# Kernel optimization log

Hardware: AMD Instinct MI355X
Metric: run time of the kernel (lower is better)

The kernel has to match this reference:

```python
import jax, jax.numpy as jnp
import numpy as np

N_HEAD = 16


def setup_inputs() -> dict:
    key = jax.random.key(0)
    ks = jax.random.split(key, 5)
    B, T, C = 4, 2048, 1024
    # torch Linear stored as [out,in]; we use [in,out] so x @ W matches x @ W_t.T
    return {
        "x": jax.random.normal(ks[0], (B, T, C), jnp.float32),
        "c_attn_w": jax.random.normal(ks[1], (C, 3 * C), jnp.float32) * 0.02,
        "c_attn_b": jax.random.normal(ks[2], (3 * C,), jnp.float32) * 0.02,
        "c_proj_w": jax.random.normal(ks[3], (C, C), jnp.float32) * 0.02,
        "c_proj_b": jax.random.normal(ks[4], (C,), jnp.float32) * 0.02,
    }


def reference(x, c_attn_w, c_attn_b, c_proj_w, c_proj_b):
    B, T, C = x.shape
    H = N_HEAD
    d = C // H
    qkv = x @ c_attn_w + c_attn_b                      # [B,T,3C]
    q, k, v = jnp.split(qkv, 3, axis=2)
    q = q.reshape(B, T, H, d).transpose(0, 2, 1, 3)    # [B,H,T,d]
    k = k.reshape(B, T, H, d).transpose(0, 2, 1, 3)
    v = v.reshape(B, T, H, d).transpose(0, 2, 1, 3)
    scale = 1.0 / jnp.sqrt(jnp.asarray(d, x.dtype))
    w = jnp.einsum("bhqd,bhkd->bhqk", q, k) * scale    # [B,H,T,T]
    causal = jnp.tril(jnp.ones((T, T), bool))
    w = jnp.where(causal, w, jnp.asarray(-jnp.inf, w.dtype))
    w = jax.nn.softmax(w, axis=-1)
    y = jnp.einsum("bhqk,bhkd->bhqd", w, v)            # [B,H,T,d]
    y = y.transpose(0, 2, 1, 3).reshape(B, T, C)
    return y @ c_proj_w + c_proj_b
```

## Files before the change

kernel.cpp:

```cpp
#include <hip/hip_runtime.h>
#include <hip/hip_bf16.h>
#include <stdint.h>

#define DEV __device__ __forceinline__

typedef __attribute__((ext_vector_type(8))) short short8;
typedef __attribute__((ext_vector_type(8))) _Float16 half8;
typedef __attribute__((ext_vector_type(2))) __fp16 fp16x2;
typedef __attribute__((ext_vector_type(4))) float floatx4;
typedef __attribute__((ext_vector_type(16))) float floatx16;

DEV unsigned short f2bf(float f) {
  union { float f; uint32_t u; } v; v.f = f;
  uint32_t u = v.u;
  u += 0x7fffu + ((u >> 16) & 1u);
  return (unsigned short)(u >> 16);
}
DEV unsigned short f2h(float f) {
  union { _Float16 h; unsigned short u; } c; c.h = (_Float16)f; return c.u;
}
DEV void async_cp16(const unsigned short* g, unsigned short* l) {
  __builtin_amdgcn_global_load_lds(
      (const __attribute__((address_space(1))) uint32_t*)g,
      (__attribute__((address_space(3))) uint32_t*)l, 16, 0, 0);
}

__global__ __launch_bounds__(256)
void cvt_x_kernel(const float* __restrict__ x, unsigned short* __restrict__ xb) {
  const size_t i = ((size_t)blockIdx.x * 256 + threadIdx.x) * 4;
  const float4 f = *(const float4*)(x + i);
  ushort4 w;
  w.x = f2bf(f.x); w.y = f2bf(f.y); w.z = f2bf(f.z); w.w = f2bf(f.w);
  *(ushort4*)(xb + i) = w;
}

__global__ __launch_bounds__(256)
void transpose_w_kernel(const float* __restrict__ W, unsigned short* __restrict__ Wt,
                        int K, int N) {
  __shared__ float tile[64][65];
  const int k0 = blockIdx.y * 64, n0 = blockIdx.x * 64;
  const int tr = threadIdx.x >> 4;
  const int tc = (threadIdx.x & 15) * 4;
#pragma unroll
  for (int it = 0; it < 4; ++it) {
    const int k = tr + it * 16;
    const float4 f = *(const float4*)(W + (size_t)(k0 + k) * N + n0 + tc);
    tile[k][tc + 0] = f.x; tile[k][tc + 1] = f.y;
    tile[k][tc + 2] = f.z; tile[k][tc + 3] = f.w;
  }
  __syncthreads();
#pragma unroll
  for (int it = 0; it < 4; ++it) {
    const int n = tr + it * 16;
    ushort4 w;
    w.x = f2bf(tile[tc + 0][n]); w.y = f2bf(tile[tc + 1][n]);
    w.z = f2bf(tile[tc + 2][n]); w.w = f2bf(tile[tc + 3][n]);
    *(ushort4*)(Wt + (size_t)(n0 + n) * K + k0 + tc) = w;
  }
}

#define BAR asm volatile("s_barrier" ::: "memory")
#define LGK0 asm volatile("s_waitcnt lgkmcnt(0)" ::: "memory")
#define VMW(N) asm volatile("s_waitcnt vmcnt(" #N ")" ::: "memory")
#define NOW (void)0
#define NOSTG (void)0

template <int EPI, int BN>
__global__ __launch_bounds__(512, 2)
void gemm256_kernel(const unsigned short* __restrict__ A,
                    const unsigned short* __restrict__ Bt,
                    const float* __restrict__ bias, int M, int N, int K,
                    int nbx,
                    unsigned short* __restrict__ qws,
                    unsigned short* __restrict__ kws,
                    unsigned short* __restrict__ vws,
                    float* __restrict__ out) {
  (void)M;
  constexpr int NF = BN / 64;
  __shared__ __align__(16) unsigned short L[2][16384 + NF * 4096];
  const int tid = threadIdx.x;
  const int wid = tid >> 6, lane = tid & 63;
  const int quad = lane >> 4, l16 = lane & 15;
  const int wm = wid >> 2, wn = wid & 3;

  const int nwg = (int)gridDim.x;
  const int bid = (int)blockIdx.x;
  const int swz = (bid & 7) * (nwg >> 3) + (bid >> 3);
  const int bx = swz % nbx, by = swz / nbx;
  const int rowA0 = by * 256, colB0 = bx * BN;

  const int srow = tid >> 3;
  const int ksrc = (((tid & 7) ^ (srow & 7)) << 3);
  const unsigned short* pA00 = A + (size_t)(rowA0 + 0   + srow) * K + ksrc;
  const unsigned short* pA01 = A + (size_t)(rowA0 + 64  + srow) * K + ksrc;
  const unsigned short* pA10 = A + (size_t)(rowA0 + 128 + srow) * K + ksrc;
  const unsigned short* pA11 = A + (size_t)(rowA0 + 192 + srow) * K + ksrc;
  const unsigned short* pB00 = Bt + (size_t)(colB0 + 0   + srow) * K + ksrc;
  const unsigned short* pB01 = Bt + (size_t)(colB0 + 64  + srow) * K + ksrc;
  const unsigned short* pB10 =
      (BN == 256) ? Bt + (size_t)(colB0 + 128 + srow) * K + ksrc : pB00;
  const unsigned short* pB11 =
      (BN == 256) ? Bt + (size_t)(colB0 + 192 + srow) * K + ksrc : pB00;

#define STG_A0(P, T) do { async_cp16(pA00 + (T)*64, &L[P][0     + wid*512]); \
                          async_cp16(pA01 + (T)*64, &L[P][4096  + wid*512]); } while (0)
#define STG_A1(P, T) do { async_cp16(pA10 + (T)*64, &L[P][8192  + wid*512]); \
                          async_cp16(pA11 + (T)*64, &L[P][12288 + wid*512]); } while (0)
#define STG_B(P, T) do { \
    async_cp16(pB00 + (T)*64, &L[P][16384 + wid*512]); \
    async_cp16(pB01 + (T)*64, &L[P][20480 + wid*512]); \
    if constexpr (BN == 256) { \
      async_cp16(pB10 + (T)*64, &L[P][24576 + wid*512]); \
      async_cp16(pB11 + (T)*64, &L[P][28672 + wid*512]); } } while (0)
#define VMW_STEADY do { if constexpr (BN == 256) { VMW(4); } else { VMW(2); } } while (0)

  floatx4 acc[8][NF];
#pragma unroll
  for (int i = 0; i < 8; ++i)
#pragma unroll
    for (int j = 0; j < NF; ++j) acc[i][j] = (floatx4){0.f, 0.f, 0.f, 0.f};
  short8 bfrag[NF];

  STG_A0(0, 0); STG_A1(0, 0); STG_B(0, 0);
  STG_B(1, 1);
  VMW_STEADY;
  BAR;

#define PHASE(PAR, QM, KS, RB, STG, W)                                        \
  {                                                                           \
    short8 a_[4];                                                             \
    _Pragma("unroll") for (int m_ = 0; m_ < 4; ++m_) {                        \
      const int row_ = wm * 128 + ((QM)*4 + m_) * 16 + l16;                   \
      a_[m_] = *(const short8*)&L[PAR][row_ * 64 +                            \
                 ((((KS)*32) + quad * 8) ^ ((row_ & 7) << 3))];               \
    }                                                                         \
    if (RB) {                                                                 \
      _Pragma("unroll") for (int n_ = 0; n_ < NF; ++n_) {                     \
        const int row_ = wn * (BN / 4) + n_ * 16 + l16;                       \
        bfrag[n_] = *(const short8*)&L[PAR][16384 + row_ * 64 +               \
                 ((((KS)*32) + quad * 8) ^ ((row_ & 7) << 3))];               \
      }                                                                       \
    }                                                                         \
    STG;                                                                      \
    BAR;                                                                      \
    LGK0;                                                                     \
    __builtin_amdgcn_s_setprio(1);                                            \
    _Pragma("unroll") for (int m_ = 0; m_ < 4; ++m_)                          \
      _Pragma("unroll") for (int n_ = 0; n_ < NF; ++n_)                       \
        acc[(QM)*4 + m_][n_] = __builtin_amdgcn_mfma_f32_16x16x32_bf16(       \
            a_[m_], bfrag[n_], acc[(QM)*4 + m_][n_], 0, 0, 0);                \
    __builtin_amdgcn_s_setprio(0);                                            \
    W;                                                                        \
    BAR;                                                                      \
  }

#define KTILE(PAR, S1, S2, S4, W4) \
  PHASE(PAR, 0, 0, 1, S1, NOW)     \
  PHASE(PAR, 1, 0, 0, S2, NOW)     \
  PHASE(PAR, 0, 1, 1, NOSTG, NOW)  \
  PHASE(PAR, 1, 1, 0, S4, W4)

  for (int t0 = 0; t0 < 14; t0 += 2) {
    KTILE(0, STG_A0(1, t0 + 1), STG_A1(1, t0 + 1), STG_B(0, t0 + 2), VMW_STEADY)
    KTILE(1, STG_A0(0, t0 + 2), STG_A1(0, t0 + 2), STG_B(1, t0 + 3), VMW_STEADY)
  }
  KTILE(0, STG_A0(1, 15), STG_A1(1, 15), NOSTG, VMW(0))
  KTILE(1, NOSTG, NOSTG, NOSTG, NOW)

#undef KTILE
#undef PHASE
#undef STG_A0
#undef STG_A1
#undef STG_B
#undef VMW_STEADY

#pragma unroll
  for (int mi = 0; mi < 8; ++mi) {
#pragma unroll
    for (int ni = 0; ni < NF; ++ni) {
      const int row0 = rowA0 + wm * 128 + mi * 16 + quad * 4;
      const int col = colB0 + wn * (BN / 4) + ni * 16 + l16;
      const float bv = bias[col];
#pragma unroll
      for (int r = 0; r < 4; ++r) {
        const float v = acc[mi][ni][r] + bv;
        const int R = row0 + r;
        if constexpr (EPI == 0) {
          const int b = R >> 11, t = R & 2047;
          const int which = col >> 10, c = col & 1023;
          const int h = c >> 6, dd = c & 63;
          const size_t bh = (size_t)(b * 16 + h);
          if (which == 0)
            qws[(bh * 2048 + t) * 64 + dd] = f2bf(v * 0.125f);
          else if (which == 1)
            kws[(bh * 2048 + t) * 64 + dd] = f2bf(v);
          else
            vws[(bh * 64 + dd) * 2048 + t] = f2h(v);
        } else {
          out[(size_t)R * N + col] = v;
        }
      }
    }
  }
}

__global__ __launch_bounds__(256, 2)
void attn_mfma_kernel(const unsigned short* __restrict__ qws,
                      const unsigned short* __restrict__ kws,
                      const unsigned short* __restrict__ vws,
                      unsigned short* __restrict__ yws) {
  constexpr int T = 2048, D = 64;
  __shared__ __align__(16) unsigned short Ks[128 * 72];
  __shared__ __align__(16) unsigned short Vs[64 * 136];
  const int tid = threadIdx.x;
  const int wid = tid >> 6, lane = tid & 63;
  const int hf = lane >> 5, l32 = lane & 31;
  const int bh = blockIdx.x;
  const int qt = 15 - (int)blockIdx.y;
  const int qbase = qt * 128;
  const unsigned short* Qp = qws + (size_t)bh * T * D;
  const unsigned short* Kp = kws + (size_t)bh * T * D;
  const unsigned short* Vp = vws + (size_t)bh * D * T;

  const int q = qbase + wid * 32 + l32;
  short8 qf[4];
#pragma unroll
  for (int s = 0; s < 4; ++s)
    qf[s] = *(const short8*)(Qp + (size_t)q * D + s * 16 + hf * 8);

  floatx16 Oacc[2];
#pragma unroll
  for (int mt2 = 0; mt2 < 2; ++mt2)
#pragma unroll
    for (int i = 0; i < 16; ++i) Oacc[mt2][i] = 0.f;
  float mrun = -1e30f, lrun = 0.f;

  for (int kt = 0; kt <= qt; ++kt) {
    const int kb = kt * 128;
    __syncthreads();
#pragma unroll
    for (int it = 0; it < 4; ++it) {
      const int e = it * 256 + tid;
      {
        const int row = e >> 3, c = (e & 7) * 8;
        *(short8*)&Ks[row * 72 + c] =
            *(const short8*)(Kp + (size_t)(kb + row) * D + c);
      }
      {
        const int row = e >> 4, c = (e & 15) * 8;
        *(short8*)&Vs[row * 136 + c] =
            *(const short8*)(Vp + (size_t)row * T + kb + c);
      }
    }
    __syncthreads();

    const bool diag = (kt == qt);
    const int mtmax = diag ? (wid + 1) : 4;

    floatx16 S[4];
#pragma unroll
    for (int mt = 0; mt < 4; ++mt)
      if (mt < mtmax)
#pragma unroll
        for (int i = 0; i < 16; ++i) S[mt][i] = 0.f;

#pragma unroll
    for (int s = 0; s < 4; ++s) {
#pragma unroll
      for (int mt = 0; mt < 4; ++mt)
        if (mt < mtmax) {
          const short8 kf =
              *(const short8*)&Ks[(mt * 32 + l32) * 72 + s * 16 + hf * 8];
          S[mt] = __builtin_amdgcn_mfma_f32_32x32x16_bf16(kf, qf[s], S[mt], 0, 0, 0);
        }
    }

    if (diag) {
#pragma unroll
      for (int mt = 0; mt < 4; ++mt)
        if (mt == wid) {
#pragma unroll
          for (int r = 0; r < 16; ++r) {
            const int intra = (r & 3) + 8 * (r >> 2) + 4 * hf;
            if (intra > l32) S[mt][r] = -1e30f;
          }
        }
    }

    float tmax = -1e30f;
#pragma unroll
    for (int mt = 0; mt < 4; ++mt)
      if (mt < mtmax)
#pragma unroll
        for (int r = 0; r < 16; ++r) tmax = fmaxf(tmax, S[mt][r]);
    tmax = fmaxf(tmax, __shfl_xor(tmax, 32, 64));
    const float mn = fmaxf(mrun, tmax);
    const float alpha = __expf(mrun - mn);
    mrun = mn;

    float tsum = 0.f;
    uint32_t pk[4][8];
#pragma unroll
    for (int mt = 0; mt < 4; ++mt)
      if (mt < mtmax)
#pragma unroll
        for (int t = 0; t < 8; ++t) {
          const float pa = __expf(S[mt][2 * t] - mn);
          const float pb = __expf(S[mt][2 * t + 1] - mn);
          tsum += pa + pb;
          union { fp16x2 h; uint32_t u; } cv;
          cv.h = __builtin_amdgcn_cvt_pkrtz(pa, pb);
          pk[mt][t] = cv.u;
        }
    tsum += __shfl_xor(tsum, 32, 64);
    lrun = lrun * alpha + tsum;
#pragma unroll
    for (int mt2 = 0; mt2 < 2; ++mt2)
#pragma unroll
      for (int i = 0; i < 16; ++i) Oacc[mt2][i] *= alpha;

    const int smax = 2 * mtmax;
#pragma unroll
    for (int s = 0; s < 8; ++s)
      if (s < smax) {
        const int mt = s >> 1;
        const int bo = 4 * (s & 1);
        const uint32_t own0 = hf ? pk[mt][bo + 2] : pk[mt][bo];
        const uint32_t own1 = hf ? pk[mt][bo + 3] : pk[mt][bo + 1];
        const uint32_t sendA = hf ? pk[mt][bo] : pk[mt][bo + 2];
        const uint32_t sendB = hf ? pk[mt][bo + 1] : pk[mt][bo + 3];
        const uint32_t recvA = (uint32_t)__shfl_xor((int)sendA, 32, 64);
        const uint32_t recvB = (uint32_t)__shfl_xor((int)sendB, 32, 64);
        union { uint32_t u[4]; half8 h; } bb;
        bb.u[0] = hf ? recvA : own0;
        bb.u[1] = hf ? recvB : own1;
        bb.u[2] = hf ? own0 : recvA;
        bb.u[3] = hf ? own1 : recvB;
#pragma unroll
        for (int mt2 = 0; mt2 < 2; ++mt2) {
          const half8 vf =
              *(const half8*)&Vs[(mt2 * 32 + l32) * 136 + s * 16 + hf * 8];
          Oacc[mt2] = __builtin_amdgcn_mfma_f32_32x32x16_f16(vf, bb.h, Oacc[mt2], 0, 0, 0);
        }
      }
  }

  const float invl = 1.0f / lrun;
  const int b_ = bh >> 4, h_ = bh & 15;
  unsigned short* yrow = yws + ((size_t)(b_ * 2048 + q)) * 1024 + h_ * 64;
#pragma unroll
  for (int mt2 = 0; mt2 < 2; ++mt2)
#pragma unroll
    for (int t = 0; t < 8; ++t) {
      const int d0 = mt2 * 32 + 2 * (t & 1) + 8 * (t >> 1) + 4 * hf;
      const uint32_t ua = f2bf(Oacc[mt2][2 * t] * invl);
      const uint32_t ub = f2bf(Oacc[mt2][2 * t + 1] * invl);
      *(uint32_t*)&yrow[d0] = ua | (ub << 16);
    }
}

extern "C" void kernel_launch(void* const* d_in, const int* in_sizes, int n_in,
                              void* d_out, int out_size, void* d_ws, size_t ws_size,
                              hipStream_t stream) {
  (void)in_sizes; (void)n_in; (void)out_size;
  const float* x = (const float*)d_in[0];
  const float* attn_w = (const float*)d_in[1];
  const float* attn_b = (const float*)d_in[2];
  const float* proj_w = (const float*)d_in[3];
  const float* proj_b = (const float*)d_in[4];
  float* out = (float*)d_out;

  const size_t NQ = 8388608;
  unsigned short* qws = (unsigned short*)d_ws;
  unsigned short* kws = qws + NQ;
  unsigned short* vws = kws + NQ;
  unsigned short* yws = vws + NQ;
  unsigned short* xb  = yws + NQ;
  unsigned short* wta = xb + NQ;
  unsigned short* wtp = wta + 3072 * 1024;
  if (ws_size < (5 * NQ + 4 * 1024 * 1024) * sizeof(unsigned short)) return;

  cvt_x_kernel<<<dim3(8192), dim3(256), 0, stream>>>(x, xb);
  transpose_w_kernel<<<dim3(48, 16), dim3(256), 0, stream>>>(attn_w, wta, 1024, 3072);
  transpose_w_kernel<<<dim3(16, 16), dim3(256), 0, stream>>>(proj_w, wtp, 1024, 1024);

  gemm256_kernel<0, 256><<<dim3(384), dim3(512), 0, stream>>>(
      xb, wta, attn_b, 8192, 3072, 1024, 12, qws, kws, vws, nullptr);
  attn_mfma_kernel<<<dim3(64, 16), dim3(256), 0, stream>>>(qws, kws, vws, yws);
  gemm256_kernel<1, 128><<<dim3(256), dim3(512), 0, stream>>>(
      yws, wtp, proj_b, 8192, 1024, 1024, 8, nullptr, nullptr, nullptr, out);
}
```

Baseline: 273.5 us.

## Halve GEMM K-tile to 32 to shrink LDS and raise occupancy

Shrinks the GEMM's per-stage K tile from 64 to 32, which halves the LDS buffers, and restructures the staging, swizzle and phase schedule to match: two phases per K-tile and twice as many iterations. Launch bounds now request 4 blocks per CU instead of 2, aiming for more resident waves to hide latency. In exchange there are twice as many barriers and waitcnt points per unit of work. The higher occupancy target may also force register spills given the 8xNF accumulator array.

```diff
diff --git a/kernel.cpp b/kernel.cpp
--- a/kernel.cpp
+++ b/kernel.cpp
@@ -66,7 +66,7 @@
 #define NOSTG (void)0
 
 template <int EPI, int BN>
-__global__ __launch_bounds__(512, 2)
+__global__ __launch_bounds__(512, 4)
 void gemm256_kernel(const unsigned short* __restrict__ A,
                     const unsigned short* __restrict__ Bt,
                     const float* __restrict__ bias, int M, int N, int K,
@@ -77,7 +77,7 @@
                     float* __restrict__ out) {
   (void)M;
   constexpr int NF = BN / 64;
-  __shared__ __align__(16) unsigned short L[2][16384 + NF * 4096];
+  __shared__ __align__(16) unsigned short L[2][8192 + NF * 2048];
   const int tid = threadIdx.x;
   const int wid = tid >> 6, lane = tid & 63;
   const int quad = lane >> 4, l16 = lane & 15;
@@ -89,30 +89,21 @@
   const int bx = swz % nbx, by = swz / nbx;
   const int rowA0 = by * 256, colB0 = bx * BN;
 
-  const int srow = tid >> 3;
-  const int ksrc = (((tid & 7) ^ (srow & 7)) << 3);
-  const unsigned short* pA00 = A + (size_t)(rowA0 + 0   + srow) * K + ksrc;
-  const unsigned short* pA01 = A + (size_t)(rowA0 + 64  + srow) * K + ksrc;
-  const unsigned short* pA10 = A + (size_t)(rowA0 + 128 + srow) * K + ksrc;
-  const unsigned short* pA11 = A + (size_t)(rowA0 + 192 + srow) * K + ksrc;
-  const unsigned short* pB00 = Bt + (size_t)(colB0 + 0   + srow) * K + ksrc;
-  const unsigned short* pB01 = Bt + (size_t)(colB0 + 64  + srow) * K + ksrc;
-  const unsigned short* pB10 =
-      (BN == 256) ? Bt + (size_t)(colB0 + 128 + srow) * K + ksrc : pB00;
-  const unsigned short* pB11 =
-      (BN == 256) ? Bt + (size_t)(colB0 + 192 + srow) * K + ksrc : pB00;
-
-#define STG_A0(P, T) do { async_cp16(pA00 + (T)*64, &L[P][0     + wid*512]); \
-                          async_cp16(pA01 + (T)*64, &L[P][4096  + wid*512]); } while (0)
-#define STG_A1(P, T) do { async_cp16(pA10 + (T)*64, &L[P][8192  + wid*512]); \
-                          async_cp16(pA11 + (T)*64, &L[P][12288 + wid*512]); } while (0)
+  const int srow = tid >> 2;
+  const int ksrc = (((tid & 3) ^ ((tid >> 4) & 3)) << 3);
+  const unsigned short* pA0 = A + (size_t)(rowA0 + srow) * K + ksrc;
+  const unsigned short* pA1 = A + (size_t)(rowA0 + 128 + srow) * K + ksrc;
+  const unsigned short* pB0 = Bt + (size_t)(colB0 + srow) * K + ksrc;
+  const unsigned short* pB1 =
+      (BN == 256) ? Bt + (size_t)(colB0 + 128 + srow) * K + ksrc : pB0;
+
+#define STG_A(P, T) do { async_cp16(pA0 + (T)*32, &L[P][0    + wid*512]); \
+                         async_cp16(pA1 + (T)*32, &L[P][4096 + wid*512]); } while (0)
 #define STG_B(P, T) do { \
-    async_cp16(pB00 + (T)*64, &L[P][16384 + wid*512]); \
-    async_cp16(pB01 + (T)*64, &L[P][20480 + wid*512]); \
+    async_cp16(pB0 + (T)*32, &L[P][8192 + wid*512]); \
     if constexpr (BN == 256) { \
-      async_cp16(pB10 + (T)*64, &L[P][24576 + wid*512]); \
-      async_cp16(pB11 + (T)*64, &L[P][28672 + wid*512]); } } while (0)
-#define VMW_STEADY do { if constexpr (BN == 256) { VMW(4); } else { VMW(2); } } while (0)
+      async_cp16(pB1 + (T)*32, &L[P][12288 + wid*512]); } } while (0)
+#define VMW_STEADY do { if constexpr (BN == 256) { VMW(2); } else { VMW(1); } } while (0)
 
   floatx4 acc[8][NF];
 #pragma unroll
@@ -121,24 +112,24 @@
     for (int j = 0; j < NF; ++j) acc[i][j] = (floatx4){0.f, 0.f, 0.f, 0.f};
   short8 bfrag[NF];
 
-  STG_A0(0, 0); STG_A1(0, 0); STG_B(0, 0);
+  const int rslot = (quad ^ (l16 >> 2)) << 3;
+
+  STG_A(0, 0); STG_B(0, 0);
   STG_B(1, 1);
   VMW_STEADY;
   BAR;
 
-#define PHASE(PAR, QM, KS, RB, STG, W)                                        \
+#define PHASE(PAR, QM, RB, STG, W)                                            \
   {                                                                           \
     short8 a_[4];                                                             \
     _Pragma("unroll") for (int m_ = 0; m_ < 4; ++m_) {                        \
       const int row_ = wm * 128 + ((QM)*4 + m_) * 16 + l16;                   \
-      a_[m_] = *(const short8*)&L[PAR][row_ * 64 +                            \
-                 ((((KS)*32) + quad * 8) ^ ((row_ & 7) << 3))];               \
+      a_[m_] = *(const short8*)&L[PAR][row_ * 32 + rslot];                    \
     }                                                                         \
     if (RB) {                                                                 \
       _Pragma("unroll") for (int n_ = 0; n_ < NF; ++n_) {                     \
         const int row_ = wn * (BN / 4) + n_ * 16 + l16;                       \
-        bfrag[n_] = *(const short8*)&L[PAR][16384 + row_ * 64 +               \
-                 ((((KS)*32) + quad * 8) ^ ((row_ & 7) << 3))];               \
+        bfrag[n_] = *(const short8*)&L[PAR][8192 + row_ * 32 + rslot];        \
       }                                                                       \
     }                                                                         \
     STG;                                                                      \
@@ -154,23 +145,20 @@
     BAR;                                                                      \
   }
 
-#define KTILE(PAR, S1, S2, S4, W4) \
-  PHASE(PAR, 0, 0, 1, S1, NOW)     \
-  PHASE(PAR, 1, 0, 0, S2, NOW)     \
-  PHASE(PAR, 0, 1, 1, NOSTG, NOW)  \
-  PHASE(PAR, 1, 1, 0, S4, W4)
-
-  for (int t0 = 0; t0 < 14; t0 += 2) {
-    KTILE(0, STG_A0(1, t0 + 1), STG_A1(1, t0 + 1), STG_B(0, t0 + 2), VMW_STEADY)
-    KTILE(1, STG_A0(0, t0 + 2), STG_A1(0, t0 + 2), STG_B(1, t0 + 3), VMW_STEADY)
-  }
-  KTILE(0, STG_A0(1, 15), STG_A1(1, 15), NOSTG, VMW(0))
-  KTILE(1, NOSTG, NOSTG, NOSTG, NOW)
+#define KTILE(PAR, S1, S2, W2) \
+  PHASE(PAR, 0, 1, S1, NOW)    \
+  PHASE(PAR, 1, 0, S2, W2)
+
+  for (int t0 = 0; t0 < 30; t0 += 2) {
+    KTILE(0, STG_A(1, t0 + 1), STG_B(0, t0 + 2), VMW_STEADY)
+    KTILE(1, STG_A(0, t0 + 2), STG_B(1, t0 + 3), VMW_STEADY)
+  }
+  KTILE(0, STG_A(1, 31), NOSTG, VMW(0))
+  KTILE(1, NOSTG, NOSTG, NOW)
 
 #undef KTILE
 #undef PHASE
-#undef STG_A0
-#undef STG_A1
+#undef STG_A
 #undef STG_B
 #undef VMW_STEADY
 
```

Measured after the change: 833.7 us. 205% more time.
